# Kernel optimization log

Measured on AMD Instinct MI355X. Metric: run time of the kernel, lower is better.

## Reference

```python
import jax, jax.numpy as jnp
import numpy as np

E, H, I, K = 8, 1024, 768, 2
T = 2048  # flattened batch*seq tokens

def setup_inputs() -> dict:
    key = jax.random.key(0)
    k1, k2, k3, k4, k5 = jax.random.split(key, 5)
    hidden_states = jax.random.normal(k1, (T, H), dtype=jnp.float32)
    gate_up_proj = jax.random.normal(k2, (E, 2 * I, H), dtype=jnp.float32) * 0.02
    down_proj = jax.random.normal(k3, (E, H, I), dtype=jnp.float32) * 0.02
    top_k_index = jax.random.randint(k4, (T, K), 0, E)
    top_k_weights = jax.nn.softmax(jax.random.normal(k5, (T, K), dtype=jnp.float32), axis=-1)
    return {
        "hidden_states": hidden_states,
        "gate_up_proj": gate_up_proj,
        "down_proj": down_proj,
        "top_k_index": top_k_index,
        "top_k_weights": top_k_weights,
    }


def reference(hidden_states, gate_up_proj, down_proj, top_k_index, top_k_weights):
    # hidden_states: [T, H]; gate_up_proj: [E, 2I, H]; down_proj: [E, H, I]
    # top_k_index: [T, K] int; top_k_weights: [T, K] float
    num_experts = gate_up_proj.shape[0]
    # Combine weights per (token, expert): zero for unrouted experts, so the
    # dense-over-experts compute below yields exactly the routed MoE output.
    onehot = jax.nn.one_hot(top_k_index, num_experts, dtype=hidden_states.dtype)  # [T, K, E]
    combine = jnp.einsum("tke,tk->te", onehot, top_k_weights)  # [T, E]
    # Grouped GEMM 1: fused gate+up projection for all experts.
    gu = jnp.einsum("th,eoh->teo", hidden_states, gate_up_proj)  # [T, E, 2I]
    inter = gu.shape[-1] // 2
    gate, up = gu[..., :inter], gu[..., inter:]
    h = jax.nn.silu(gate) * up  # [T, E, I]
    # Grouped GEMM 2: down projection.
    expert_out = jnp.einsum("tei,ehi->teh", h, down_proj)  # [T, E, H]
    return jnp.einsum("teh,te->th", expert_out, combine)  # [T, H]
```

## Files before the change

kernel.cpp:

```cpp
#include <hip/hip_runtime.h>
#include <hip/hip_bf16.h>

#define T_TOK   2048
#define NEXP    8
#define HDIM    1024
#define IDIM    768
#define TOPK    2
#define NASSIGN (T_TOK*TOPK)
#define MT      64
#define MAX_TILES 72
#define SLOT_PAD 4608

typedef unsigned short u16;
typedef unsigned int   u32;

typedef __bf16 bf16x8 __attribute__((ext_vector_type(8)));
typedef float  f32x4  __attribute__((ext_vector_type(4)));

struct Meta {
  int n_tiles;
  int _pad[15];
  int tile_e[80];
  int tile_m[80];
  int tile_n[80];
};

__device__ __forceinline__ u16 f2bf(float f) {
  u32 x = __float_as_uint(f);
  return (u16)((x + 0x7fffu + ((x >> 16) & 1u)) >> 16);
}

__device__ __forceinline__ int4 pack8(const float* __restrict__ p) {
  float4 a = *(const float4*)p;
  float4 b = *(const float4*)(p + 4);
  union { u16 u[8]; int4 v; } r;
  r.u[0] = f2bf(a.x); r.u[1] = f2bf(a.y); r.u[2] = f2bf(a.z); r.u[3] = f2bf(a.w);
  r.u[4] = f2bf(b.x); r.u[5] = f2bf(b.y); r.u[6] = f2bf(b.z); r.u[7] = f2bf(b.w);
  return r.v;
}

__device__ __forceinline__ bf16x8 asbf(int4 v) {
  return __builtin_bit_cast(bf16x8, v);
}

__device__ __forceinline__ void gll(const void* g, void* l) {
  __builtin_amdgcn_global_load_lds(
      (const __attribute__((address_space(1))) u32*)g,
      (__attribute__((address_space(3))) u32*)l, 16, 0, 0);
}

__global__ __launch_bounds__(256) void prep_k(
    const float* __restrict__ hs, const float* __restrict__ gup,
    const float* __restrict__ down, const int* __restrict__ topk,
    const float* __restrict__ tw,
    u16* __restrict__ hs16, u16* __restrict__ gup16, u16* __restrict__ down16,
    Meta* __restrict__ meta, int* __restrict__ slot_token, float* __restrict__ slot_w,
    float* __restrict__ out) {
  int tid = threadIdx.x;

  if (blockIdx.x == 0) {
    __shared__ int s_cnt[NEXP], s_off[NEXP], s_cur[NEXP];
    if (tid < NEXP) { s_cnt[tid] = 0; s_cur[tid] = 0; }
    __syncthreads();
    for (int i = tid; i < NASSIGN; i += 256)
      atomicAdd(&s_cnt[topk[i]], 1);
    __syncthreads();
    if (tid == 0) {
      int acc = 0, nt = 0;
      for (int e = 0; e < NEXP; ++e) {
        s_off[e] = acc;
        int c = s_cnt[e];
        for (int mb = 0; mb < c; mb += MT) {
          meta->tile_e[nt] = e;
          meta->tile_m[nt] = acc + mb;
          meta->tile_n[nt] = (c - mb) < MT ? (c - mb) : MT;
          ++nt;
        }
        acc += c;
      }
      meta->n_tiles = nt;
    }
    __syncthreads();
    for (int i = tid; i < NASSIGN; i += 256) {
      int e = topk[i];
      int p = s_off[e] + atomicAdd(&s_cur[e], 1);
      slot_token[p] = i / TOPK;
      slot_w[p]     = tw[i];
    }
    for (int i = NASSIGN + tid; i < SLOT_PAD; i += 256) {
      slot_token[i] = 0;
      slot_w[i]     = 0.0f;
    }
    return;
  }

  const size_t NG_GUP = (size_t)NEXP * 2 * IDIM * HDIM / 8;
  const size_t NG_DWN = (size_t)NEXP * HDIM * IDIM / 8;
  const size_t NG_HS  = (size_t)T_TOK * HDIM / 8;
  const size_t NG_OUT = (size_t)T_TOK * HDIM / 4;
  size_t gid    = ((size_t)(blockIdx.x - 1) * 256 + tid) * 2;
  size_t stride = (size_t)(gridDim.x - 1) * 256 * 2;

  for (size_t g = gid; g < NG_GUP; g += stride) {
    *(int4*)(gup16 + g * 8)     = pack8(gup + g * 8);
    *(int4*)(gup16 + g * 8 + 8) = pack8(gup + g * 8 + 8);
  }
  for (size_t g = gid; g < NG_DWN; g += stride) {
    *(int4*)(down16 + g * 8)     = pack8(down + g * 8);
    *(int4*)(down16 + g * 8 + 8) = pack8(down + g * 8 + 8);
  }
  for (size_t g = gid; g < NG_HS; g += stride) {
    *(int4*)(hs16 + g * 8)     = pack8(hs + g * 8);
    *(int4*)(hs16 + g * 8 + 8) = pack8(hs + g * 8 + 8);
  }
  int4 z = {0, 0, 0, 0};
  for (size_t g = gid; g < NG_OUT; g += stride) {
    *(int4*)(out + g * 4)     = z;
    *(int4*)(out + g * 4 + 4) = z;
  }
}

__global__ __launch_bounds__(256, 2) void gemm1_k(
    const u16* __restrict__ hs16, const u16* __restrict__ gup16,
    const Meta* __restrict__ meta, const int* __restrict__ slot_token,
    const float* __restrict__ slot_w, u16* __restrict__ hbuf) {
  int bid = blockIdx.x;
  int wg = (bid & 7) * 108 + (bid >> 3);
  int tile = wg / 12, y = wg % 12;
  if (tile >= meta->n_tiles) return;
  int e = meta->tile_e[tile], mbase = meta->tile_m[tile], nrows = meta->tile_n[tile];
  int n0 = y * 64;

  __shared__ int4 lds[3][3][512];
  int tid = threadIdx.x, lane = tid & 63, w = tid >> 6, wm = w >> 1, wn = w & 1;
  f32x4 accg[2][2] = {}, accu[2][2] = {};

  const u16* gb = gup16 + (size_t)e * (2 * IDIM) * HDIM + (size_t)n0 * HDIM;
  const u16* ub = gb + (size_t)IDIM * HDIM;

  int c0 = tid, c1 = tid + 256;
  int r0 = c0 >> 3, s0 = (c0 & 7) ^ (r0 & 7);
  int r1 = c1 >> 3, s1 = (c1 & 7) ^ (r1 & 7);
  const u16* a0 = hs16 + (size_t)slot_token[mbase + r0] * HDIM + s0 * 8;
  const u16* a1 = hs16 + (size_t)slot_token[mbase + r1] * HDIM + s1 * 8;
  const u16* g0 = gb + (size_t)r0 * HDIM + s0 * 8;
  const u16* g1 = gb + (size_t)r1 * HDIM + s1 * 8;
  const u16* u0 = ub + (size_t)r0 * HDIM + s0 * 8;
  const u16* u1 = ub + (size_t)r1 * HDIM + s1 * 8;

  auto STAGE = [&](int b, int k0) {
    gll(a0 + k0, &lds[b][0][w * 64]);
    gll(a1 + k0, &lds[b][0][256 + w * 64]);
    gll(g0 + k0, &lds[b][1][w * 64]);
    gll(g1 + k0, &lds[b][1][256 + w * 64]);
    gll(u0 + k0, &lds[b][2][w * 64]);
    gll(u1 + k0, &lds[b][2][256 + w * 64]);
  };

  STAGE(0, 0);
  STAGE(1, 64);
  #pragma unroll
  for (int kt = 0; kt < 16; ++kt) {
    __builtin_amdgcn_s_barrier();
    if (kt + 2 < 16) STAGE((kt + 2) % 3, (kt + 2) * 64);
    if (kt < 14)       asm volatile("s_waitcnt vmcnt(12)" ::: "memory");
    else if (kt == 14) asm volatile("s_waitcnt vmcnt(6)" ::: "memory");
    else               asm volatile("s_waitcnt vmcnt(0)" ::: "memory");
    __builtin_amdgcn_sched_barrier(0);
    const int cur = kt % 3;
    #pragma unroll
    for (int ks = 0; ks < 2; ++ks) {
      bf16x8 af[2], bgf[2], buf_[2];
      int slot = ks * 4 + (lane >> 4);
      #pragma unroll
      for (int i = 0; i < 2; ++i) {
        int row = wm * 32 + i * 16 + (lane & 15);
        af[i] = asbf(lds[cur][0][(row << 3) | (slot ^ (row & 7))]);
      }
      #pragma unroll
      for (int j = 0; j < 2; ++j) {
        int row = wn * 32 + j * 16 + (lane & 15);
        int idx = (row << 3) | (slot ^ (row & 7));
        bgf[j]  = asbf(lds[cur][1][idx]);
        buf_[j] = asbf(lds[cur][2][idx]);
      }
      #pragma unroll
      for (int i = 0; i < 2; ++i)
        #pragma unroll
        for (int j = 0; j < 2; ++j) {
          accg[i][j] = __builtin_amdgcn_mfma_f32_16x16x32_bf16(af[i], bgf[j],  accg[i][j], 0, 0, 0);
          accu[i][j] = __builtin_amdgcn_mfma_f32_16x16x32_bf16(af[i], buf_[j], accu[i][j], 0, 0, 0);
        }
    }
  }

  int fq = lane >> 4, fr = lane & 15;
  #pragma unroll
  for (int i = 0; i < 2; ++i)
    #pragma unroll
    for (int r = 0; r < 4; ++r) {
      int row = wm * 32 + i * 16 + fq * 4 + r;
      if (row < nrows) {
        float wgt = slot_w[mbase + row];
        #pragma unroll
        for (int j = 0; j < 2; ++j) {
          float g = accg[i][j][r], u = accu[i][j][r];
          float s = g / (1.0f + __expf(-g));
          hbuf[(size_t)(mbase + row) * IDIM + n0 + wn * 32 + j * 16 + fr] = f2bf(s * u * wgt);
        }
      }
    }
}

__global__ __launch_bounds__(256, 3) void gemm2_k(
    const u16* __restrict__ hbuf, const u16* __restrict__ down16,
    const Meta* __restrict__ meta, const int* __restrict__ slot_token,
    float* __restrict__ out) {
  int bid = blockIdx.x;
  int wg = (bid & 7) * 144 + (bid >> 3);
  int tile = wg / 16, y = wg % 16;
  if (tile >= meta->n_tiles) return;
  int e = meta->tile_e[tile], mbase = meta->tile_m[tile], nrows = meta->tile_n[tile];
  int n0 = y * 64;

  __shared__ int4 lds[3][2][512];
  int tid = threadIdx.x, lane = tid & 63, w = tid >> 6, wm = w >> 1, wn = w & 1;
  f32x4 acc[2][2] = {};
  const u16* db = down16 + (size_t)e * HDIM * IDIM + (size_t)n0 * IDIM;

  int c0 = tid, c1 = tid + 256;
  int r0 = c0 >> 3, s0 = (c0 & 7) ^ (r0 & 7);
  int r1 = c1 >> 3, s1 = (c1 & 7) ^ (r1 & 7);
  const u16* a0 = hbuf + (size_t)(mbase + r0) * IDIM + s0 * 8;
  const u16* a1 = hbuf + (size_t)(mbase + r1) * IDIM + s1 * 8;
  const u16* b0 = db + (size_t)r0 * IDIM + s0 * 8;
  const u16* b1 = db + (size_t)r1 * IDIM + s1 * 8;

  auto STAGE = [&](int b, int k0) {
    gll(a0 + k0, &lds[b][0][w * 64]);
    gll(a1 + k0, &lds[b][0][256 + w * 64]);
    gll(b0 + k0, &lds[b][1][w * 64]);
    gll(b1 + k0, &lds[b][1][256 + w * 64]);
  };

  STAGE(0, 0);
  STAGE(1, 64);
  #pragma unroll
  for (int kt = 0; kt < 12; ++kt) {
    __builtin_amdgcn_s_barrier();
    if (kt + 2 < 12) STAGE((kt + 2) % 3, (kt + 2) * 64);
    if (kt < 10)       asm volatile("s_waitcnt vmcnt(8)" ::: "memory");
    else if (kt == 10) asm volatile("s_waitcnt vmcnt(4)" ::: "memory");
    else               asm volatile("s_waitcnt vmcnt(0)" ::: "memory");
    __builtin_amdgcn_sched_barrier(0);
    const int cur = kt % 3;
    #pragma unroll
    for (int ks = 0; ks < 2; ++ks) {
      bf16x8 af[2], bf[2];
      int slot = ks * 4 + (lane >> 4);
      #pragma unroll
      for (int i = 0; i < 2; ++i) {
        int row = wm * 32 + i * 16 + (lane & 15);
        af[i] = asbf(lds[cur][0][(row << 3) | (slot ^ (row & 7))]);
      }
      #pragma unroll
      for (int j = 0; j < 2; ++j) {
        int row = wn * 32 + j * 16 + (lane & 15);
        bf[j] = asbf(lds[cur][1][(row << 3) | (slot ^ (row & 7))]);
      }
      #pragma unroll
      for (int i = 0; i < 2; ++i)
        #pragma unroll
        for (int j = 0; j < 2; ++j)
          acc[i][j] = __builtin_amdgcn_mfma_f32_16x16x32_bf16(af[i], bf[j], acc[i][j], 0, 0, 0);
    }
  }

  int fq = lane >> 4, fr = lane & 15;
  #pragma unroll
  for (int i = 0; i < 2; ++i)
    #pragma unroll
    for (int r = 0; r < 4; ++r) {
      int row = wm * 32 + i * 16 + fq * 4 + r;
      if (row < nrows) {
        int tok = slot_token[mbase + row];
        #pragma unroll
        for (int j = 0; j < 2; ++j)
          atomicAdd(out + (size_t)tok * HDIM + n0 + wn * 32 + j * 16 + fr, acc[i][j][r]);
      }
    }
}

extern "C" void kernel_launch(void* const* d_in, const int* in_sizes, int n_in,
                              void* d_out, int out_size, void* d_ws, size_t ws_size,
                              hipStream_t stream) {
  const float* hs   = (const float*)d_in[0];
  const float* gup  = (const float*)d_in[1];
  const float* down = (const float*)d_in[2];
  const int*   topk = (const int*)d_in[3];
  const float* tw   = (const float*)d_in[4];
  float* out = (float*)d_out;

  const size_t o_hs16   = 65536;
  const size_t o_hbuf   = o_hs16 + (size_t)T_TOK * HDIM * 2;
  const size_t o_gup16  = o_hbuf + (size_t)SLOT_PAD * IDIM * 2;
  const size_t o_down16 = o_gup16 + (size_t)NEXP * 2 * IDIM * HDIM * 2;
  const size_t needed   = o_down16 + (size_t)NEXP * HDIM * IDIM * 2;

  char* ws = (char*)d_ws;
  Meta*  meta       = (Meta*)ws;
  int*   slot_token = (int*)(ws + 4096);
  float* slot_w     = (float*)(ws + 24576);
  u16*   hs16       = (u16*)(ws + o_hs16);
  u16*   hbuf       = (u16*)(ws + o_hbuf);
  u16*   gup16      = (u16*)(ws + o_gup16);
  u16*   down16     = (u16*)(ws + o_down16);

  if (ws_size < needed) return;

  prep_k<<<4096, 256, 0, stream>>>(hs, gup, down, topk, tw,
                                   hs16, gup16, down16, meta, slot_token, slot_w, out);
  gemm1_k<<<MAX_TILES * 12, 256, 0, stream>>>(hs16, gup16, meta, slot_token, slot_w, hbuf);
  gemm2_k<<<MAX_TILES * 16, 256, 0, stream>>>(hbuf, down16, meta, slot_token, out);
}
```

Before: 178.7 us.

## Enlarge GEMM tiles to 128x128 with 512-thread blocks and fixed-count prep loops

Doubles the routed-token tile (MT 64→128) and output tile width to 128 in both grouped GEMMs, using 8 waves per 512-thread block so each wave owns a 64x32 sub-tile. This raises data reuse per LDS load and halves the number of weight re-reads across M tiles. gemm2 also drops from triple to double buffering, and the prep kernel uses 513 blocks with fully unrolled fixed-count conversion loops instead of a grid-stride loop. The risks are more padding waste per expert, fewer blocks to fill the CUs, and less latency hiding from the shallower gemm2 pipeline.

```diff
diff --git a/kernel.cpp b/kernel.cpp
--- a/kernel.cpp
+++ b/kernel.cpp
@@ -7,9 +7,9 @@
 #define IDIM    768
 #define TOPK    2
 #define NASSIGN (T_TOK*TOPK)
-#define MT      64
-#define MAX_TILES 72
-#define SLOT_PAD 4608
+#define MT      128
+#define MAX_TILES 40
+#define SLOT_PAD 5120
 
 typedef unsigned short u16;
 typedef unsigned int   u32;
@@ -94,51 +94,52 @@
     return;
   }
 
-  const size_t NG_GUP = (size_t)NEXP * 2 * IDIM * HDIM / 8;
-  const size_t NG_DWN = (size_t)NEXP * HDIM * IDIM / 8;
-  const size_t NG_HS  = (size_t)T_TOK * HDIM / 8;
-  const size_t NG_OUT = (size_t)T_TOK * HDIM / 4;
-  size_t gid    = ((size_t)(blockIdx.x - 1) * 256 + tid) * 2;
-  size_t stride = (size_t)(gridDim.x - 1) * 256 * 2;
-
-  for (size_t g = gid; g < NG_GUP; g += stride) {
-    *(int4*)(gup16 + g * 8)     = pack8(gup + g * 8);
-    *(int4*)(gup16 + g * 8 + 8) = pack8(gup + g * 8 + 8);
-  }
-  for (size_t g = gid; g < NG_DWN; g += stride) {
-    *(int4*)(down16 + g * 8)     = pack8(down + g * 8);
-    *(int4*)(down16 + g * 8 + 8) = pack8(down + g * 8 + 8);
-  }
-  for (size_t g = gid; g < NG_HS; g += stride) {
-    *(int4*)(hs16 + g * 8)     = pack8(hs + g * 8);
-    *(int4*)(hs16 + g * 8 + 8) = pack8(hs + g * 8 + 8);
+  const size_t NTH = 512 * 256;
+  size_t t = ((size_t)blockIdx.x - 1) * 256 + tid;
+
+  #pragma unroll
+  for (int k = 0; k < 12; ++k) {
+    size_t i = t + (size_t)k * NTH;
+    *(int4*)(gup16 + i * 8) = pack8(gup + i * 8);
+  }
+  #pragma unroll
+  for (int k = 0; k < 6; ++k) {
+    size_t i = t + (size_t)k * NTH;
+    *(int4*)(down16 + i * 8) = pack8(down + i * 8);
+  }
+  #pragma unroll
+  for (int k = 0; k < 2; ++k) {
+    size_t i = t + (size_t)k * NTH;
+    *(int4*)(hs16 + i * 8) = pack8(hs + i * 8);
   }
   int4 z = {0, 0, 0, 0};
-  for (size_t g = gid; g < NG_OUT; g += stride) {
-    *(int4*)(out + g * 4)     = z;
-    *(int4*)(out + g * 4 + 4) = z;
-  }
-}
-
-__global__ __launch_bounds__(256, 2) void gemm1_k(
+  #pragma unroll
+  for (int k = 0; k < 4; ++k) {
+    size_t i = t + (size_t)k * NTH;
+    *(int4*)(out + i * 4) = z;
+  }
+}
+
+__global__ __launch_bounds__(512, 2) void gemm1_k(
     const u16* __restrict__ hs16, const u16* __restrict__ gup16,
     const Meta* __restrict__ meta, const int* __restrict__ slot_token,
     const float* __restrict__ slot_w, u16* __restrict__ hbuf) {
   int bid = blockIdx.x;
-  int wg = (bid & 7) * 108 + (bid >> 3);
-  int tile = wg / 12, y = wg % 12;
+  int wg = (bid & 7) * 30 + (bid >> 3);
+  int tile = wg / 6, y = wg % 6;
   if (tile >= meta->n_tiles) return;
   int e = meta->tile_e[tile], mbase = meta->tile_m[tile], nrows = meta->tile_n[tile];
-  int n0 = y * 64;
-
-  __shared__ int4 lds[3][3][512];
-  int tid = threadIdx.x, lane = tid & 63, w = tid >> 6, wm = w >> 1, wn = w & 1;
-  f32x4 accg[2][2] = {}, accu[2][2] = {};
+  int n0 = y * 128;
+
+  __shared__ int4 lds[3][3][1024];
+  int tid = threadIdx.x, lane = tid & 63, w = tid >> 6;
+  int wm = w >> 2, wn = w & 3;
+  f32x4 accg[4][2] = {}, accu[4][2] = {};
 
   const u16* gb = gup16 + (size_t)e * (2 * IDIM) * HDIM + (size_t)n0 * HDIM;
   const u16* ub = gb + (size_t)IDIM * HDIM;
 
-  int c0 = tid, c1 = tid + 256;
+  int c0 = tid, c1 = tid + 512;
   int r0 = c0 >> 3, s0 = (c0 & 7) ^ (r0 & 7);
   int r1 = c1 >> 3, s1 = (c1 & 7) ^ (r1 & 7);
   const u16* a0 = hs16 + (size_t)slot_token[mbase + r0] * HDIM + s0 * 8;
@@ -150,11 +151,11 @@
 
   auto STAGE = [&](int b, int k0) {
     gll(a0 + k0, &lds[b][0][w * 64]);
-    gll(a1 + k0, &lds[b][0][256 + w * 64]);
+    gll(a1 + k0, &lds[b][0][512 + w * 64]);
     gll(g0 + k0, &lds[b][1][w * 64]);
-    gll(g1 + k0, &lds[b][1][256 + w * 64]);
+    gll(g1 + k0, &lds[b][1][512 + w * 64]);
     gll(u0 + k0, &lds[b][2][w * 64]);
-    gll(u1 + k0, &lds[b][2][256 + w * 64]);
+    gll(u1 + k0, &lds[b][2][512 + w * 64]);
   };
 
   STAGE(0, 0);
@@ -170,11 +171,11 @@
     const int cur = kt % 3;
     #pragma unroll
     for (int ks = 0; ks < 2; ++ks) {
-      bf16x8 af[2], bgf[2], buf_[2];
+      bf16x8 af[4], bgf[2], buf_[2];
       int slot = ks * 4 + (lane >> 4);
       #pragma unroll
-      for (int i = 0; i < 2; ++i) {
-        int row = wm * 32 + i * 16 + (lane & 15);
+      for (int i = 0; i < 4; ++i) {
+        int row = wm * 64 + i * 16 + (lane & 15);
         af[i] = asbf(lds[cur][0][(row << 3) | (slot ^ (row & 7))]);
       }
       #pragma unroll
@@ -185,7 +186,7 @@
         buf_[j] = asbf(lds[cur][2][idx]);
       }
       #pragma unroll
-      for (int i = 0; i < 2; ++i)
+      for (int i = 0; i < 4; ++i)
         #pragma unroll
         for (int j = 0; j < 2; ++j) {
           accg[i][j] = __builtin_amdgcn_mfma_f32_16x16x32_bf16(af[i], bgf[j],  accg[i][j], 0, 0, 0);
@@ -196,10 +197,10 @@
 
   int fq = lane >> 4, fr = lane & 15;
   #pragma unroll
-  for (int i = 0; i < 2; ++i)
+  for (int i = 0; i < 4; ++i)
     #pragma unroll
     for (int r = 0; r < 4; ++r) {
-      int row = wm * 32 + i * 16 + fq * 4 + r;
+      int row = wm * 64 + i * 16 + fq * 4 + r;
       if (row < nrows) {
         float wgt = slot_w[mbase + row];
         #pragma unroll
@@ -212,23 +213,24 @@
     }
 }
 
-__global__ __launch_bounds__(256, 3) void gemm2_k(
+__global__ __launch_bounds__(512, 4) void gemm2_k(
     const u16* __restrict__ hbuf, const u16* __restrict__ down16,
     const Meta* __restrict__ meta, const int* __restrict__ slot_token,
     float* __restrict__ out) {
   int bid = blockIdx.x;
-  int wg = (bid & 7) * 144 + (bid >> 3);
-  int tile = wg / 16, y = wg % 16;
+  int wg = (bid & 7) * 40 + (bid >> 3);
+  int tile = wg / 8, y = wg % 8;
   if (tile >= meta->n_tiles) return;
   int e = meta->tile_e[tile], mbase = meta->tile_m[tile], nrows = meta->tile_n[tile];
-  int n0 = y * 64;
-
-  __shared__ int4 lds[3][2][512];
-  int tid = threadIdx.x, lane = tid & 63, w = tid >> 6, wm = w >> 1, wn = w & 1;
-  f32x4 acc[2][2] = {};
+  int n0 = y * 128;
+
+  __shared__ int4 lds[2][2][1024];
+  int tid = threadIdx.x, lane = tid & 63, w = tid >> 6;
+  int wm = w >> 2, wn = w & 3;
+  f32x4 acc[4][2] = {};
   const u16* db = down16 + (size_t)e * HDIM * IDIM + (size_t)n0 * IDIM;
 
-  int c0 = tid, c1 = tid + 256;
+  int c0 = tid, c1 = tid + 512;
   int r0 = c0 >> 3, s0 = (c0 & 7) ^ (r0 & 7);
   int r1 = c1 >> 3, s1 = (c1 & 7) ^ (r1 & 7);
   const u16* a0 = hbuf + (size_t)(mbase + r0) * IDIM + s0 * 8;
@@ -238,29 +240,27 @@
 
   auto STAGE = [&](int b, int k0) {
     gll(a0 + k0, &lds[b][0][w * 64]);
-    gll(a1 + k0, &lds[b][0][256 + w * 64]);
+    gll(a1 + k0, &lds[b][0][512 + w * 64]);
     gll(b0 + k0, &lds[b][1][w * 64]);
-    gll(b1 + k0, &lds[b][1][256 + w * 64]);
+    gll(b1 + k0, &lds[b][1][512 + w * 64]);
   };
 
   STAGE(0, 0);
-  STAGE(1, 64);
   #pragma unroll
   for (int kt = 0; kt < 12; ++kt) {
     __builtin_amdgcn_s_barrier();
-    if (kt + 2 < 12) STAGE((kt + 2) % 3, (kt + 2) * 64);
-    if (kt < 10)       asm volatile("s_waitcnt vmcnt(8)" ::: "memory");
-    else if (kt == 10) asm volatile("s_waitcnt vmcnt(4)" ::: "memory");
-    else               asm volatile("s_waitcnt vmcnt(0)" ::: "memory");
+    if (kt + 1 < 12) STAGE((kt + 1) & 1, (kt + 1) * 64);
+    if (kt < 11) asm volatile("s_waitcnt vmcnt(4)" ::: "memory");
+    else         asm volatile("s_waitcnt vmcnt(0)" ::: "memory");
     __builtin_amdgcn_sched_barrier(0);
-    const int cur = kt % 3;
+    const int cur = kt & 1;
     #pragma unroll
     for (int ks = 0; ks < 2; ++ks) {
-      bf16x8 af[2], bf[2];
+      bf16x8 af[4], bf[2];
       int slot = ks * 4 + (lane >> 4);
       #pragma unroll
-      for (int i = 0; i < 2; ++i) {
-        int row = wm * 32 + i * 16 + (lane & 15);
+      for (int i = 0; i < 4; ++i) {
+        int row = wm * 64 + i * 16 + (lane & 15);
         af[i] = asbf(lds[cur][0][(row << 3) | (slot ^ (row & 7))]);
       }
       #pragma unroll
@@ -269,7 +269,7 @@
         bf[j] = asbf(lds[cur][1][(row << 3) | (slot ^ (row & 7))]);
       }
       #pragma unroll
-      for (int i = 0; i < 2; ++i)
+      for (int i = 0; i < 4; ++i)
         #pragma unroll
         for (int j = 0; j < 2; ++j)
           acc[i][j] = __builtin_amdgcn_mfma_f32_16x16x32_bf16(af[i], bf[j], acc[i][j], 0, 0, 0);
@@ -278,10 +278,10 @@
 
   int fq = lane >> 4, fr = lane & 15;
   #pragma unroll
-  for (int i = 0; i < 2; ++i)
+  for (int i = 0; i < 4; ++i)
     #pragma unroll
     for (int r = 0; r < 4; ++r) {
-      int row = wm * 32 + i * 16 + fq * 4 + r;
+      int row = wm * 64 + i * 16 + fq * 4 + r;
       if (row < nrows) {
         int tok = slot_token[mbase + row];
         #pragma unroll
@@ -318,8 +318,8 @@
 
   if (ws_size < needed) return;
 
-  prep_k<<<4096, 256, 0, stream>>>(hs, gup, down, topk, tw,
-                                   hs16, gup16, down16, meta, slot_token, slot_w, out);
-  gemm1_k<<<MAX_TILES * 12, 256, 0, stream>>>(hs16, gup16, meta, slot_token, slot_w, hbuf);
-  gemm2_k<<<MAX_TILES * 16, 256, 0, stream>>>(hbuf, down16, meta, slot_token, out);
-}
+  prep_k<<<513, 256, 0, stream>>>(hs, gup, down, topk, tw,
+                                  hs16, gup16, down16, meta, slot_token, slot_w, out);
+  gemm1_k<<<MAX_TILES * 6, 512, 0, stream>>>(hs16, gup16, meta, slot_token, slot_w, hbuf);
+  gemm2_k<<<MAX_TILES * 8, 512, 0, stream>>>(hbuf, down16, meta, slot_token, out);
+}
```

New measurement: 177.7 us. About the same (-0.5%).
